# Optimization experiments

Measured on AMD Instinct MI355X. Metric: run time of the kernel, lower is better.

The kernel has to match this reference:

```python
import jax, jax.numpy as jnp
import numpy as np

VOCAB, EMB, HID, OUT = 1000, 256, 512, 1
NUM_IN, NUM_OUT = 7, 4
B, S = 64, 512
D = EMB + NUM_OUT  # conv input dim = 260


def setup_inputs() -> dict:
    key = jax.random.key(0)
    ks = jax.random.split(key, 8)
    ev = jax.random.randint(ks[0], (B, S, 1), 0, VOCAB).astype(jnp.float32)
    num = jax.random.normal(ks[1], (B, S, NUM_IN), jnp.float32)
    X = jnp.concatenate([ev, num], axis=-1)  # [B,S,8]; col 0 = event ids
    def w(k, shape, fan_in):
        return jax.random.normal(k, shape, jnp.float32) / np.sqrt(fan_in).astype(np.float32)
    return {
        "X": X,
        "emb": w(ks[2], (VOCAB, EMB), EMB),
        "Wn": w(ks[3], (NUM_IN, NUM_OUT), NUM_IN), "bn": jnp.zeros((NUM_OUT,), jnp.float32),
        "Wf": w(ks[4], (D, 3 * HID), D), "bf": jnp.zeros((3 * HID,), jnp.float32),
        "Wb": w(ks[5], (D, 3 * HID), D), "bb": jnp.zeros((3 * HID,), jnp.float32),
        "Wo": w(ks[6], (2 * HID, OUT), 2 * HID), "bo": jnp.zeros((OUT,), jnp.float32),
    }


def _fo_pool(Z, F):
    # Z, F: [S, B, H]. Linear recurrence h_t = F_t * h_{t-1} + (1 - F_t) * Z_t.
    def step(h, zf):
        z, f = zf
        h = f * h + (1.0 - f) * z
        return h, h
    h0 = jnp.zeros(Z.shape[1:], Z.dtype)
    _, hs = jax.lax.scan(step, h0, (Z, F))
    return hs  # [S, B, H]


def _forward(X, emb, Wn, bn, Wf, bf, Wb, bb, Wo, bo):
    ev = jax.lax.stop_gradient(X[:, :, 0]).astype(jnp.int32)  # event-type ids
    num = X[:, :, 1:]
    e = emb[ev]                          # [B,S,EMB]
    n = num @ Wn + bn                    # [B,S,NUM_OUT]
    c = jnp.concatenate([e, n], axis=-1)  # [B,S,D]

    def gates(W, b):
        g = jnp.einsum('bsd,dk->sbk', c, W) + b  # kernel-1 conv == GEMM; [S,B,3H]
        Z, F = g[..., :HID], g[..., HID:2 * HID]  # O gate is computed but unused upstream
        return jnp.tanh(Z), jax.nn.sigmoid(F)

    Zf, Ff = gates(Wf, bf)
    Zb, Fb = gates(Wb, bb)
    hf = _fo_pool(Zf, Ff)                       # forward direction
    hb = _fo_pool(Zb[::-1], Fb[::-1])[::-1]     # backward: scan reversed, re-reverse
    # torch takes h_combined[-1]: last forward state, first backward-scan state
    final = jnp.concatenate([hf[-1], hb[-1]], axis=-1)  # [B, 2H]
    return final @ Wo + bo  # dropout p=0 is identity


def reference(X, emb, Wn, bn, Wf, bf, Wb, bb, Wo, bo):
    return _forward(X, emb, Wn, bn, Wf, bf, Wb, bb, Wo, bo)
```

## Files before the change

### kernel.cpp

```cpp
#include <hip/hip_runtime.h>
#include <stdint.h>

#define B_ 64
#define S_ 512
#define EMB_ 256
#define NIN_ 7
#define NOUT_ 4
#define HID_ 512
#define VOCAB_ 1000
#define VP_ 1024
#define NG_ 2048
#define M_ (B_ * S_)

typedef __bf16 bf16x8 __attribute__((ext_vector_type(8)));
typedef float floatx4 __attribute__((ext_vector_type(4)));
typedef unsigned short u16x8 __attribute__((ext_vector_type(8)));

__device__ __forceinline__ unsigned short f2bf(float f) {
    unsigned u = __float_as_uint(f);
    u += 0x7FFFu + ((u >> 16) & 1u);
    return (unsigned short)(u >> 16);
}
__device__ __forceinline__ float bf2f(unsigned short h) {
    return __uint_as_float(((unsigned)h) << 16);
}
__device__ __forceinline__ float rcp_(float x) { return __builtin_amdgcn_rcpf(x); }
__device__ __forceinline__ float sigmoidf_(float x) {
    return rcp_(1.0f + __expf(-x));
}
__device__ __forceinline__ float tanhf_(float x) {
    float ax = fabsf(x);
    float e = __expf(-2.0f * ax);
    float t = (1.0f - e) * rcp_(1.0f + e);
    return copysignf(t, x);
}


__global__ __launch_bounds__(256) void prep(
    const float* __restrict__ emb, const float* __restrict__ Wn,
    const float* __restrict__ bn, const float* __restrict__ Wf,
    const float* __restrict__ bfv, const float* __restrict__ Wb,
    const float* __restrict__ bb,
    unsigned short* __restrict__ Aemb, unsigned short* __restrict__ WT,
    float* __restrict__ W7, float* __restrict__ bvec) {
    int bid = blockIdx.x;
    int tid = threadIdx.x;

    if (bid < 64) {
        int g = bid;
#pragma unroll
        for (int half = 0; half < 2; ++half) {
            int t = tid + 256 * half;
            int r15 = t & 15;
            int kchunk = (t >> 4) & 3;
            int kt = t >> 6;
            int row = g * 16 + r15;
            int k0 = kt * 32 + kchunk * 8;
            unsigned short p[8];
            if (row < VOCAB_) {
                float4 a = *(const float4*)(emb + (size_t)row * EMB_ + k0);
                float4 b = *(const float4*)(emb + (size_t)row * EMB_ + k0 + 4);
                p[0]=f2bf(a.x); p[1]=f2bf(a.y); p[2]=f2bf(a.z); p[3]=f2bf(a.w);
                p[4]=f2bf(b.x); p[5]=f2bf(b.y); p[6]=f2bf(b.z); p[7]=f2bf(b.w);
            } else {
#pragma unroll
                for (int q = 0; q < 8; ++q) p[q] = 0;
            }
            size_t chunk = ((size_t)(g >> 3) * 8 + kt) * 8 + (g & 7);
            *(u16x8*)(Aemb + chunk * 512 + (16 * kchunk + r15) * 8) =
                *(const u16x8*)p;
        }
    } else if (bid < 192) {
        int g = bid - 64;
#pragma unroll
        for (int half = 0; half < 2; ++half) {
            int t = tid + 256 * half;
            int v15 = t & 15;
            int kchunk = (t >> 4) & 3;
            int kt = t >> 6;
            int v = g * 16 + v15;
            int part = v >> 10;
            int m = v & 1023;
            int j = m >> 1;
            int c = (m & 1) ? (512 + j) : j;
            const float* W = part ? Wb : Wf;
            int k0 = kt * 32 + kchunk * 8;
            unsigned short p[8];
#pragma unroll
            for (int q = 0; q < 8; ++q)
                p[q] = f2bf(W[(size_t)(k0 + q) * 1536 + c]);
            size_t chunk = ((size_t)(g >> 3) * 8 + kt) * 8 + (g & 7);
            *(u16x8*)(WT + chunk * 512 + (16 * kchunk + v15) * 8) =
                *(const u16x8*)p;
        }
    } else {
        float wn[NIN_][NOUT_];
#pragma unroll
        for (int i = 0; i < NIN_; ++i)
#pragma unroll
            for (int q = 0; q < NOUT_; ++q) wn[i][q] = Wn[i * NOUT_ + q];
        float bnr[NOUT_];
#pragma unroll
        for (int q = 0; q < NOUT_; ++q) bnr[q] = bn[q];
#pragma unroll
        for (int it = 0; it < 8; ++it) {
            int v = tid + 256 * it;
            int part = v >> 10;
            int m = v & 1023;
            int j = m >> 1;
            int c = (m & 1) ? (512 + j) : j;
            const float* W = part ? Wb : Wf;
            float wnum[NOUT_];
#pragma unroll
            for (int q = 0; q < NOUT_; ++q)
                wnum[q] = W[(size_t)(256 + q) * 1536 + c];
            float bv = part ? bb[c] : bfv[c];
#pragma unroll
            for (int q = 0; q < NOUT_; ++q) bv += bnr[q] * wnum[q];
            bvec[v] = bv;
#pragma unroll
            for (int i = 0; i < NIN_; ++i) {
                float s = 0.f;
#pragma unroll
                for (int q = 0; q < NOUT_; ++q) s += wn[i][q] * wnum[q];
                W7[(size_t)i * NG_ + v] = s;
            }
        }
    }
}

__global__ __launch_bounds__(256) void gemmG(
    const unsigned short* __restrict__ Aemb, const unsigned short* __restrict__ WT,
    const float* __restrict__ bvec, unsigned short* __restrict__ G) {
    int bid = blockIdx.x;
    int mtile = bid & 7;
    int ntile = bid >> 3;
    int r0 = mtile * 128;
    int n0 = ntile * 128;
    int tid = threadIdx.x;
    int lane = tid & 63, wave = tid >> 6;
    int wm = wave & 1, wn = wave >> 1;
    int rl = lane & 15;

    const unsigned short* pa = Aemb + ((size_t)mtile * 64 + 4 * wm) * 512 + lane * 8;
    const unsigned short* pb = WT + ((size_t)ntile * 64 + 4 * wn) * 512 + lane * 8;

    floatx4 acc[4][4];
#pragma unroll
    for (int mi = 0; mi < 4; ++mi)
#pragma unroll
        for (int ni = 0; ni < 4; ++ni) acc[mi][ni] = (floatx4){0.f, 0.f, 0.f, 0.f};

    bf16x8 afc[4], bfc[4], afn[4], bfn[4];
#pragma unroll
    for (int mi = 0; mi < 4; ++mi) afc[mi] = *(const bf16x8*)(pa + mi * 512);
#pragma unroll
    for (int ni = 0; ni < 4; ++ni) bfc[ni] = *(const bf16x8*)(pb + ni * 512);

#pragma unroll
    for (int kt = 0; kt < 8; ++kt) {
        if (kt < 7) {
#pragma unroll
            for (int mi = 0; mi < 4; ++mi)
                afn[mi] = *(const bf16x8*)(pa + (size_t)(kt + 1) * 4096 + mi * 512);
#pragma unroll
            for (int ni = 0; ni < 4; ++ni)
                bfn[ni] = *(const bf16x8*)(pb + (size_t)(kt + 1) * 4096 + ni * 512);
        }
#pragma unroll
        for (int mi = 0; mi < 4; ++mi)
#pragma unroll
            for (int ni = 0; ni < 4; ++ni)
                acc[mi][ni] = __builtin_amdgcn_mfma_f32_16x16x32_bf16(afc[mi], bfc[ni], acc[mi][ni], 0, 0, 0);
        if (kt < 7) {
#pragma unroll
            for (int mi = 0; mi < 4; ++mi) afc[mi] = afn[mi];
#pragma unroll
            for (int ni = 0; ni < 4; ++ni) bfc[ni] = bfn[ni];
        }
    }

#pragma unroll
    for (int ni = 0; ni < 4; ++ni) {
        int n = n0 + 64 * wn + 16 * ni + rl;
        float bv = bvec[n];
#pragma unroll
        for (int mi = 0; mi < 4; ++mi) {
            int rb = r0 + 64 * wm + 16 * mi + (lane >> 4) * 4;
#pragma unroll
            for (int v = 0; v < 4; ++v)
                G[(size_t)(rb + v) * NG_ + n] = f2bf(acc[mi][ni][v] + bv);
        }
    }
}

__global__ __launch_bounds__(512) void scan(
    const float* __restrict__ X, const unsigned short* __restrict__ G,
    const float* __restrict__ W7, float* __restrict__ PQ) {
    __shared__ float LX[512];
    int bid = blockIdx.x;
    int b = bid >> 3, chunk = bid & 7;
    int s0 = chunk * 64;
    int j = threadIdx.x;

    LX[j] = X[((size_t)b * S_ + s0 + (j >> 3)) * 8 + (j & 7)];
    __syncthreads();

    float2 w7p[NIN_];
#pragma unroll
    for (int i = 0; i < NIN_; ++i)
        w7p[i] = *(const float2*)(W7 + (size_t)i * NG_ + 2 * j);

    float P = 1.f, Q = 0.f;
    int ev0 = (int)LX[0];
    unsigned gp = *(const unsigned*)(G + (size_t)ev0 * NG_ + 2 * j);
#pragma unroll 4
    for (int s = 0; s < 64; ++s) {
        unsigned gpc = gp;
        if (s < 63) {
            int evn = (int)LX[(s + 1) * 8];
            gp = *(const unsigned*)(G + (size_t)evn * NG_ + 2 * j);
        }
        float gz = bf2f((unsigned short)(gpc & 0xffffu));
        float gf = bf2f((unsigned short)(gpc >> 16));
#pragma unroll
        for (int i = 0; i < NIN_; ++i) {
            float x = LX[s * 8 + 1 + i];
            gz += x * w7p[i].x;
            gf += x * w7p[i].y;
        }
        float z = tanhf_(gz);
        float f = sigmoidf_(gf);
        Q = f * Q + (1.f - f) * z;
        P *= f;
    }
    ((float2*)PQ)[(size_t)bid * 512 + j] = make_float2(P, Q);
}

__global__ __launch_bounds__(512) void final_out(
    const float* __restrict__ X, const unsigned short* __restrict__ G,
    const float* __restrict__ W7, const float* __restrict__ Wo,
    const float* __restrict__ bo, const float* __restrict__ PQ,
    float* __restrict__ out) {
    int b = blockIdx.x;
    int j = threadIdx.x;

    float h = 0.f;
#pragma unroll
    for (int c = 0; c < 8; ++c) {
        float2 pq = ((const float2*)PQ)[((size_t)b * 8 + c) * 512 + j];
        h = pq.x * h + pq.y;
    }

    const float* xr = X + ((size_t)b * S_ + (S_ - 1)) * 8;
    int ev = (int)xr[0];
    unsigned gpc = *(const unsigned*)(G + (size_t)ev * NG_ + 1024 + 2 * j);
    float gz = bf2f((unsigned short)(gpc & 0xffffu));
    float gf = bf2f((unsigned short)(gpc >> 16));
#pragma unroll
    for (int i = 0; i < NIN_; ++i) {
        float2 w = *(const float2*)(W7 + (size_t)i * NG_ + 1024 + 2 * j);
        float x = xr[1 + i];
        gz += x * w.x;
        gf += x * w.y;
    }
    float hb = (1.f - sigmoidf_(gf)) * tanhf_(gz);

    float partial = h * Wo[j] + hb * Wo[512 + j];
    __shared__ float red[512];
    red[j] = partial;
    __syncthreads();
    for (int off = 256; off > 0; off >>= 1) {
        if (j < off) red[j] += red[j + off];
        __syncthreads();
    }
    if (j == 0) out[b] = red[0] + bo[0];
}

extern "C" void kernel_launch(void* const* d_in, const int* in_sizes, int n_in,
                              void* d_out, int out_size, void* d_ws, size_t ws_size,
                              hipStream_t stream) {
    const float* X   = (const float*)d_in[0];
    const float* emb = (const float*)d_in[1];
    const float* Wn  = (const float*)d_in[2];
    const float* bn  = (const float*)d_in[3];
    const float* Wf  = (const float*)d_in[4];
    const float* bfv = (const float*)d_in[5];
    const float* Wb  = (const float*)d_in[6];
    const float* bb  = (const float*)d_in[7];
    const float* Wo  = (const float*)d_in[8];
    const float* bo  = (const float*)d_in[9];
    float* out = (float*)d_out;

    size_t off_A  = 0;
    size_t off_WT = off_A  + (size_t)VP_ * EMB_ * 2;
    size_t off_G  = off_WT + (size_t)NG_ * EMB_ * 2;
    size_t off_W7 = off_G  + (size_t)VP_ * NG_ * 2;
    size_t off_bv = off_W7 + (size_t)NIN_ * NG_ * 4;
    size_t off_PQ = off_bv + (size_t)NG_ * 4;
    size_t need   = off_PQ + (size_t)B_ * 8 * 512 * 2 * sizeof(float);
    if (ws_size < need) return;

    unsigned short* Aemb = (unsigned short*)((char*)d_ws + off_A);
    unsigned short* WT   = (unsigned short*)((char*)d_ws + off_WT);
    unsigned short* G    = (unsigned short*)((char*)d_ws + off_G);
    float*          W7   = (float*)((char*)d_ws + off_W7);
    float*          bvec = (float*)((char*)d_ws + off_bv);
    float*          PQ   = (float*)((char*)d_ws + off_PQ);

    prep<<<193, 256, 0, stream>>>(emb, Wn, bn, Wf, bfv, Wb, bb,
                                  Aemb, WT, W7, bvec);
    gemmG<<<128, 256, 0, stream>>>(Aemb, WT, bvec, G);
    scan<<<512, 512, 0, stream>>>(X, G, W7, PQ);
    final_out<<<64, 512, 0, stream>>>(X, G, W7, Wo, bo, PQ, out);
}
```

Before: 115.0 us.

## Coalesce weight transpose via LDS, factor numeric projection, deepen gather prefetch

The weight transpose in prep now stages tiles of Wf/Wb through shared memory with float4 loads, replacing strided scalar reads, and the prep grid shrinks accordingly. The folded 7-input numeric weights are replaced by the raw 4-column slice, with the 7->4 projection computed per timestep into LDS inside scan, cutting per-step FMAs. The scan also prefetches G rows two steps ahead, and uses raw v_exp_f32 and an fma form of the recurrence. final_out switches to a wave-shuffle reduction; together these are several unrelated micro-optimizations that add a little extra per-block work in scan.

Result: faster. 109.9 us (-4.4%).

```diff
diff --git a/kernel.cpp b/kernel.cpp
--- a/kernel.cpp
+++ b/kernel.cpp
@@ -25,24 +25,27 @@
     return __uint_as_float(((unsigned)h) << 16);
 }
 __device__ __forceinline__ float rcp_(float x) { return __builtin_amdgcn_rcpf(x); }
+__device__ __forceinline__ float exp2_(float x) {
+    float r; asm("v_exp_f32 %0, %1" : "=v"(r) : "v"(x)); return r;
+}
+#define L2E_ 1.4426950408889634f
 __device__ __forceinline__ float sigmoidf_(float x) {
-    return rcp_(1.0f + __expf(-x));
+    return rcp_(1.0f + exp2_(x * (-L2E_)));
 }
 __device__ __forceinline__ float tanhf_(float x) {
     float ax = fabsf(x);
-    float e = __expf(-2.0f * ax);
+    float e = exp2_(ax * (-2.0f * L2E_));
     float t = (1.0f - e) * rcp_(1.0f + e);
     return copysignf(t, x);
 }
 
 
 __global__ __launch_bounds__(256) void prep(
-    const float* __restrict__ emb, const float* __restrict__ Wn,
-    const float* __restrict__ bn, const float* __restrict__ Wf,
-    const float* __restrict__ bfv, const float* __restrict__ Wb,
-    const float* __restrict__ bb,
+    const float* __restrict__ emb, const float* __restrict__ bn,
+    const float* __restrict__ Wf, const float* __restrict__ bfv,
+    const float* __restrict__ Wb, const float* __restrict__ bb,
     unsigned short* __restrict__ Aemb, unsigned short* __restrict__ WT,
-    float* __restrict__ W7, float* __restrict__ bvec) {
+    float* __restrict__ W4, float* __restrict__ bvec) {
     int bid = blockIdx.x;
     int tid = threadIdx.x;
 
@@ -70,62 +73,63 @@
             *(u16x8*)(Aemb + chunk * 512 + (16 * kchunk + r15) * 8) =
                 *(const u16x8*)p;
         }
-    } else if (bid < 192) {
-        int g = bid - 64;
-#pragma unroll
-        for (int half = 0; half < 2; ++half) {
-            int t = tid + 256 * half;
-            int v15 = t & 15;
-            int kchunk = (t >> 4) & 3;
-            int kt = t >> 6;
-            int v = g * 16 + v15;
-            int part = v >> 10;
-            int m = v & 1023;
-            int j = m >> 1;
-            int c = (m & 1) ? (512 + j) : j;
-            const float* W = part ? Wb : Wf;
-            int k0 = kt * 32 + kchunk * 8;
-            unsigned short p[8];
-#pragma unroll
-            for (int q = 0; q < 8; ++q)
-                p[q] = f2bf(W[(size_t)(k0 + q) * 1536 + c]);
-            size_t chunk = ((size_t)(g >> 3) * 8 + kt) * 8 + (g & 7);
-            *(u16x8*)(WT + chunk * 512 + (16 * kchunk + v15) * 8) =
-                *(const u16x8*)p;
+    } else if (bid < 80) {
+        __shared__ float raw[32][132];
+        int idx = bid - 64;
+        int p = idx >> 3;
+        int gq = idx & 7;
+        const float* W = p ? Wb : Wf;
+        int j0 = gq * 64;
+        int r = tid >> 3;
+        int i = tid & 7;
+
+#pragma unroll
+        for (int kt = 0; kt < 8; ++kt) {
+            int k0 = kt * 32;
+            const float* src = W + (size_t)(k0 + r) * 1536;
+            float4 a0 = *(const float4*)(src + j0 + i * 8);
+            float4 a1 = *(const float4*)(src + j0 + i * 8 + 4);
+            float4 b0 = *(const float4*)(src + 512 + j0 + i * 8);
+            float4 b1 = *(const float4*)(src + 512 + j0 + i * 8 + 4);
+            *(float4*)&raw[r][i * 8]      = a0;
+            *(float4*)&raw[r][i * 8 + 4]  = a1;
+            *(float4*)&raw[r][64 + i * 8]     = b0;
+            *(float4*)&raw[r][64 + i * 8 + 4] = b1;
+            __syncthreads();
+#pragma unroll
+            for (int h = 0; h < 2; ++h) {
+                int e = tid + 256 * h;
+                int gl = e >> 6;
+                int rest = e & 63;
+                int kchunk = rest >> 4;
+                int v15 = rest & 15;
+                int joff = gl * 8 + (v15 >> 1);
+                int cl = joff + 64 * (v15 & 1);
+                unsigned short pk[8];
+#pragma unroll
+                for (int q = 0; q < 8; ++q) pk[q] = f2bf(raw[kchunk * 8 + q][cl]);
+                int g = p * 64 + gq * 8 + gl;
+                size_t chunk = ((size_t)(g >> 3) * 8 + kt) * 8 + (g & 7);
+                *(u16x8*)(WT + chunk * 512 + (16 * kchunk + v15) * 8) =
+                    *(const u16x8*)pk;
+            }
+            __syncthreads();
         }
     } else {
-        float wn[NIN_][NOUT_];
-#pragma unroll
-        for (int i = 0; i < NIN_; ++i)
-#pragma unroll
-            for (int q = 0; q < NOUT_; ++q) wn[i][q] = Wn[i * NOUT_ + q];
-        float bnr[NOUT_];
-#pragma unroll
-        for (int q = 0; q < NOUT_; ++q) bnr[q] = bn[q];
-#pragma unroll
-        for (int it = 0; it < 8; ++it) {
-            int v = tid + 256 * it;
-            int part = v >> 10;
-            int m = v & 1023;
-            int j = m >> 1;
-            int c = (m & 1) ? (512 + j) : j;
-            const float* W = part ? Wb : Wf;
-            float wnum[NOUT_];
-#pragma unroll
-            for (int q = 0; q < NOUT_; ++q)
-                wnum[q] = W[(size_t)(256 + q) * 1536 + c];
-            float bv = part ? bb[c] : bfv[c];
-#pragma unroll
-            for (int q = 0; q < NOUT_; ++q) bv += bnr[q] * wnum[q];
-            bvec[v] = bv;
-#pragma unroll
-            for (int i = 0; i < NIN_; ++i) {
-                float s = 0.f;
-#pragma unroll
-                for (int q = 0; q < NOUT_; ++q) s += wn[i][q] * wnum[q];
-                W7[(size_t)i * NG_ + v] = s;
-            }
-        }
+        int v = (bid - 80) * 256 + tid;
+        int part = v >> 10;
+        int m = v & 1023;
+        int j = m >> 1;
+        int c = (m & 1) ? (512 + j) : j;
+        const float* W = part ? Wb : Wf;
+        float bv = part ? bb[c] : bfv[c];
+#pragma unroll
+        for (int q = 0; q < NOUT_; ++q) {
+            float w = W[(size_t)(256 + q) * 1536 + c];
+            W4[(size_t)q * NG_ + v] = w;
+            bv = fmaf(bn[q], w, bv);
+        }
+        bvec[v] = bv;
     }
 }
 
@@ -196,8 +200,10 @@
 
 __global__ __launch_bounds__(512) void scan(
     const float* __restrict__ X, const unsigned short* __restrict__ G,
-    const float* __restrict__ W7, float* __restrict__ PQ) {
+    const float* __restrict__ W4, const float* __restrict__ Wn,
+    float* __restrict__ PQ) {
     __shared__ float LX[512];
+    __shared__ float LN[64][4];
     int bid = blockIdx.x;
     int b = bid >> 3, chunk = bid & 7;
     int s0 = chunk * 64;
@@ -206,32 +212,47 @@
     LX[j] = X[((size_t)b * S_ + s0 + (j >> 3)) * 8 + (j & 7)];
     __syncthreads();
 
-    float2 w7p[NIN_];
-#pragma unroll
-    for (int i = 0; i < NIN_; ++i)
-        w7p[i] = *(const float2*)(W7 + (size_t)i * NG_ + 2 * j);
+    if (j < 256) {
+        int t = j >> 2, q = j & 3;
+        float s = 0.f;
+#pragma unroll
+        for (int i = 0; i < NIN_; ++i) s = fmaf(LX[t * 8 + 1 + i], Wn[i * NOUT_ + q], s);
+        LN[t][q] = s;
+    }
+
+    float2 w4p[NOUT_];
+#pragma unroll
+    for (int q = 0; q < NOUT_; ++q)
+        w4p[q] = *(const float2*)(W4 + (size_t)q * NG_ + 2 * j);
+    __syncthreads();
 
     float P = 1.f, Q = 0.f;
     int ev0 = (int)LX[0];
-    unsigned gp = *(const unsigned*)(G + (size_t)ev0 * NG_ + 2 * j);
+    unsigned gpA = *(const unsigned*)(G + (size_t)ev0 * NG_ + 2 * j);
+    int ev1 = (int)LX[8];
+    unsigned gpB = *(const unsigned*)(G + (size_t)ev1 * NG_ + 2 * j);
 #pragma unroll 4
     for (int s = 0; s < 64; ++s) {
-        unsigned gpc = gp;
-        if (s < 63) {
-            int evn = (int)LX[(s + 1) * 8];
-            gp = *(const unsigned*)(G + (size_t)evn * NG_ + 2 * j);
+        unsigned gpc = gpA;
+        gpA = gpB;
+        if (s < 62) {
+            int evn = (int)LX[(s + 2) * 8];
+            gpB = *(const unsigned*)(G + (size_t)evn * NG_ + 2 * j);
         }
         float gz = bf2f((unsigned short)(gpc & 0xffffu));
         float gf = bf2f((unsigned short)(gpc >> 16));
-#pragma unroll
-        for (int i = 0; i < NIN_; ++i) {
-            float x = LX[s * 8 + 1 + i];
-            gz += x * w7p[i].x;
-            gf += x * w7p[i].y;
-        }
+        float4 n4 = *(const float4*)(&LN[s][0]);
+        gz = fmaf(n4.x, w4p[0].x, gz);
+        gz = fmaf(n4.y, w4p[1].x, gz);
+        gz = fmaf(n4.z, w4p[2].x, gz);
+        gz = fmaf(n4.w, w4p[3].x, gz);
+        gf = fmaf(n4.x, w4p[0].y, gf);
+        gf = fmaf(n4.y, w4p[1].y, gf);
+        gf = fmaf(n4.z, w4p[2].y, gf);
+        gf = fmaf(n4.w, w4p[3].y, gf);
         float z = tanhf_(gz);
         float f = sigmoidf_(gf);
-        Q = f * Q + (1.f - f) * z;
+        Q = fmaf(f, Q - z, z);
         P *= f;
     }
     ((float2*)PQ)[(size_t)bid * 512 + j] = make_float2(P, Q);
@@ -239,9 +260,9 @@
 
 __global__ __launch_bounds__(512) void final_out(
     const float* __restrict__ X, const unsigned short* __restrict__ G,
-    const float* __restrict__ W7, const float* __restrict__ Wo,
-    const float* __restrict__ bo, const float* __restrict__ PQ,
-    float* __restrict__ out) {
+    const float* __restrict__ W4, const float* __restrict__ Wn,
+    const float* __restrict__ Wo, const float* __restrict__ bo,
+    const float* __restrict__ PQ, float* __restrict__ out) {
     int b = blockIdx.x;
     int j = threadIdx.x;
 
@@ -249,32 +270,43 @@
 #pragma unroll
     for (int c = 0; c < 8; ++c) {
         float2 pq = ((const float2*)PQ)[((size_t)b * 8 + c) * 512 + j];
-        h = pq.x * h + pq.y;
+        h = fmaf(pq.x, h, pq.y);
     }
 
     const float* xr = X + ((size_t)b * S_ + (S_ - 1)) * 8;
     int ev = (int)xr[0];
+    float n4[NOUT_];
+#pragma unroll
+    for (int q = 0; q < NOUT_; ++q) {
+        float s = 0.f;
+#pragma unroll
+        for (int i = 0; i < NIN_; ++i) s = fmaf(xr[1 + i], Wn[i * NOUT_ + q], s);
+        n4[q] = s;
+    }
     unsigned gpc = *(const unsigned*)(G + (size_t)ev * NG_ + 1024 + 2 * j);
     float gz = bf2f((unsigned short)(gpc & 0xffffu));
     float gf = bf2f((unsigned short)(gpc >> 16));
 #pragma unroll
-    for (int i = 0; i < NIN_; ++i) {
-        float2 w = *(const float2*)(W7 + (size_t)i * NG_ + 1024 + 2 * j);
-        float x = xr[1 + i];
-        gz += x * w.x;
-        gf += x * w.y;
+    for (int q = 0; q < NOUT_; ++q) {
+        float2 w = *(const float2*)(W4 + (size_t)q * NG_ + 1024 + 2 * j);
+        gz = fmaf(n4[q], w.x, gz);
+        gf = fmaf(n4[q], w.y, gf);
     }
     float hb = (1.f - sigmoidf_(gf)) * tanhf_(gz);
 
-    float partial = h * Wo[j] + hb * Wo[512 + j];
-    __shared__ float red[512];
-    red[j] = partial;
+    float partial = fmaf(h, Wo[j], hb * Wo[512 + j]);
+#pragma unroll
+    for (int off = 32; off > 0; off >>= 1)
+        partial += __shfl_down(partial, off);
+    __shared__ float red[8];
+    if ((j & 63) == 0) red[j >> 6] = partial;
     __syncthreads();
-    for (int off = 256; off > 0; off >>= 1) {
-        if (j < off) red[j] += red[j + off];
-        __syncthreads();
-    }
-    if (j == 0) out[b] = red[0] + bo[0];
+    if (j == 0) {
+        float s = bo[0];
+#pragma unroll
+        for (int w = 0; w < 8; ++w) s += red[w];
+        out[b] = s;
+    }
 }
 
 extern "C" void kernel_launch(void* const* d_in, const int* in_sizes, int n_in,
@@ -295,8 +327,8 @@
     size_t off_A  = 0;
     size_t off_WT = off_A  + (size_t)VP_ * EMB_ * 2;
     size_t off_G  = off_WT + (size_t)NG_ * EMB_ * 2;
-    size_t off_W7 = off_G  + (size_t)VP_ * NG_ * 2;
-    size_t off_bv = off_W7 + (size_t)NIN_ * NG_ * 4;
+    size_t off_W4 = off_G  + (size_t)VP_ * NG_ * 2;
+    size_t off_bv = off_W4 + (size_t)NOUT_ * NG_ * 4;
     size_t off_PQ = off_bv + (size_t)NG_ * 4;
     size_t need   = off_PQ + (size_t)B_ * 8 * 512 * 2 * sizeof(float);
     if (ws_size < need) return;
@@ -304,13 +336,12 @@
     unsigned short* Aemb = (unsigned short*)((char*)d_ws + off_A);
     unsigned short* WT   = (unsigned short*)((char*)d_ws + off_WT);
     unsigned short* G    = (unsigned short*)((char*)d_ws + off_G);
-    float*          W7   = (float*)((char*)d_ws + off_W7);
+    float*          W4   = (float*)((char*)d_ws + off_W4);
     float*          bvec = (float*)((char*)d_ws + off_bv);
     float*          PQ   = (float*)((char*)d_ws + off_PQ);
 
-    prep<<<193, 256, 0, stream>>>(emb, Wn, bn, Wf, bfv, Wb, bb,
-                                  Aemb, WT, W7, bvec);
+    prep<<<88, 256, 0, stream>>>(emb, bn, Wf, bfv, Wb, bb, Aemb, WT, W4, bvec);
     gemmG<<<128, 256, 0, stream>>>(Aemb, WT, bvec, G);
-    scan<<<512, 512, 0, stream>>>(X, G, W7, PQ);
-    final_out<<<64, 512, 0, stream>>>(X, G, W7, Wo, bo, PQ, out);
-}
+    scan<<<512, 512, 0, stream>>>(X, G, W4, Wn, PQ);
+    final_out<<<64, 512, 0, stream>>>(X, G, W4, Wn, Wo, bo, PQ, out);
+}
```
